# Kernel tuning notes

Measured on AMD Instinct MI355X. Metric: run time of the kernel, lower is better.

Reference implementation:

```python
import jax, jax.numpy as jnp
import numpy as np
from jax.ops import segment_sum, segment_max

N = 50000
E = 800000
F_IN = 128
F_HEAD = 32
HEADS = 8
N_CLASSES = 32
NEG_SLOPE = 0.2


def setup_inputs() -> dict:
    key = jax.random.key(0)
    ks = jax.random.split(key, 12)
    x = jax.random.normal(ks[0], (N, F_IN), dtype=jnp.float32)
    edge_index = jax.random.randint(ks[1], (2, E), 0, N, dtype=jnp.int64)
    # layer 1 params (in=128 -> heads=8, out=32)
    s1 = 1.0 / np.sqrt(F_IN)
    W1 = jax.random.uniform(ks[2], (F_IN, HEADS * F_HEAD), jnp.float32, -s1, s1)
    a_src1 = jax.random.uniform(ks[3], (HEADS, F_HEAD), jnp.float32, -s1, s1)
    a_dst1 = jax.random.uniform(ks[4], (HEADS, F_HEAD), jnp.float32, -s1, s1)
    b1 = jnp.zeros((HEADS * F_HEAD,), jnp.float32)
    # layer 2 params (in=256 -> heads=1, out=32)
    s2 = 1.0 / np.sqrt(HEADS * F_HEAD)
    W2 = jax.random.uniform(ks[5], (HEADS * F_HEAD, N_CLASSES), jnp.float32, -s2, s2)
    a_src2 = jax.random.uniform(ks[6], (1, N_CLASSES), jnp.float32, -s2, s2)
    a_dst2 = jax.random.uniform(ks[7], (1, N_CLASSES), jnp.float32, -s2, s2)
    b2 = jnp.zeros((N_CLASSES,), jnp.float32)
    return {"x": x, "edge_index": edge_index, "W1": W1, "a_src1": a_src1,
            "a_dst1": a_dst1, "b1": b1, "W2": W2, "a_src2": a_src2,
            "a_dst2": a_dst2, "b2": b2}


def gat_conv(x, W, a_src, a_dst, b, src, dst, heads, out_ch):
    n = x.shape[0]
    h = (x @ W).reshape(n, heads, out_ch)                  # [N,H,F]
    alpha_src = jnp.einsum('nhf,hf->nh', h, a_src)         # [N,H]
    alpha_dst = jnp.einsum('nhf,hf->nh', h, a_dst)
    e = alpha_src[src] + alpha_dst[dst]                    # [E,H]
    e = jnp.where(e > 0, e, NEG_SLOPE * e)                 # LeakyReLU(0.2)
    # segment softmax over edges grouped by destination node
    m = segment_max(e, dst, num_segments=n)                # [N,H]
    ex = jnp.exp(e - m[dst])
    denom = segment_sum(ex, dst, num_segments=n)           # [N,H]
    alpha = ex / (denom[dst] + 1e-16)                      # [E,H]
    out = segment_sum(alpha[:, :, None] * h[src], dst, num_segments=n)  # [N,H,F]
    return out.reshape(n, heads * out_ch) + b


def reference(x, edge_index, W1, a_src1, a_dst1, b1, W2, a_src2, a_dst2, b2):
    src, dst = edge_index[0], edge_index[1]
    h = gat_conv(x, W1, a_src1, a_dst1, b1, src, dst, HEADS, F_HEAD)
    h = jax.nn.elu(h)
    out = gat_conv(h, W2, a_src2, a_dst2, b2, src, dst, 1, N_CLASSES)
    return out
```

## Files before the change

### kernel.cpp

```cpp
#include <hip/hip_runtime.h>
#include <math.h>

#define NNODES 50000
#define NEDGES 800000
#define GB 782

typedef _Float16 f16;
typedef _Float16 f16x8 __attribute__((ext_vector_type(8)));
typedef _Float16 f16x4 __attribute__((ext_vector_type(4)));
typedef float f32x4 __attribute__((ext_vector_type(4)));
typedef float f32x8 __attribute__((ext_vector_type(8)));


__global__ __launch_bounds__(256) void k_deg_wfrag(const int* __restrict__ ei, int* __restrict__ deg,
                                                   int* __restrict__ rank,
                                                   const float* __restrict__ W1, const float* __restrict__ W2,
                                                   f16* __restrict__ W1f, f16* __restrict__ W2f) {
    int bid = blockIdx.x;
    if (bid < NEDGES / 256) {
        int e = bid * 256 + threadIdx.x;
        rank[e] = atomicAdd(&deg[ei[NEDGES + e]], 1);
    } else {
        int id = (bid - NEDGES / 256) * 256 + threadIdx.x;
        if (id < 32768) {
            int k = id >> 8, c = id & 255;
            int kc = k >> 5, quad = (k & 31) >> 3, j = k & 7;
            W1f[(((kc << 8) + c) * 4 + quad) * 8 + j] = (f16)W1[id];
        } else {
            int i2 = id - 32768;
            int k = i2 >> 5, c = i2 & 31;
            int kc = k >> 5, quad = (k & 31) >> 3, j = k & 7;
            W2f[(((kc << 5) + c) * 4 + quad) * 8 + j] = (f16)W2[i2];
        }
    }
}

__global__ __launch_bounds__(256) void k_scanA(const int* __restrict__ deg, int* __restrict__ incl,
                                               int* __restrict__ partial) {
    int t = threadIdx.x;
    int i = blockIdx.x * 256 + t;
    int v = (i < NNODES) ? deg[i] : 0;
    int lane = t & 63, wid = t >> 6;
    int s = v;
#pragma unroll
    for (int d = 1; d < 64; d <<= 1) { int u = __shfl_up(s, d, 64); if (lane >= d) s += u; }
    __shared__ int wtot[4];
    if (lane == 63) wtot[wid] = s;
    __syncthreads();
    int off = 0;
    for (int w = 0; w < wid; ++w) off += wtot[w];
    s += off;
    if (i < NNODES) incl[i] = s;
    if (t == 255) partial[blockIdx.x] = s;
}

__global__ __launch_bounds__(256) void k_scanC(const int* __restrict__ deg, const int* __restrict__ incl,
                                               const int* __restrict__ partial, int* __restrict__ rowst) {
    int t = threadIdx.x, bid = blockIdx.x;
    int v = (t < bid) ? partial[t] : 0;
    int lane = t & 63, wid = t >> 6;
#pragma unroll
    for (int d = 1; d < 64; d <<= 1) v += __shfl_xor(v, d);
    __shared__ int ws[4];
    if (lane == 0) ws[wid] = v;
    __syncthreads();
    int choff = ws[0] + ws[1] + ws[2] + ws[3];
    int i = bid * 256 + t;
    if (i < NNODES) {
        int rs1 = incl[i] + choff;
        rowst[i + 1] = rs1;
        if (i == 0) rowst[0] = 0;
    }
}


__global__ __launch_bounds__(256) void k_gemm1_sc(const float* __restrict__ X, const f16* __restrict__ W1f,
                                                  const float* __restrict__ Asrc, const float* __restrict__ Adst,
                                                  f16* __restrict__ h1h, float* __restrict__ as1,
                                                  float* __restrict__ ad1, const int* __restrict__ ei,
                                                  const int* __restrict__ rowst, const int* __restrict__ rank,
                                                  unsigned* __restrict__ sd_csr) {
    __shared__ f16 sA[64 * 136];
    int bid = blockIdx.x;
    int t = threadIdx.x;
    if (bid >= GB) {
        int e = (bid - GB) * 256 + t;
        if (e < NEDGES) {
            int s = ei[e], d = ei[NEDGES + e];
            int pos = rowst[d] + rank[e];
            sd_csr[pos] = ((unsigned)d << 16) | (unsigned)s;
        }
        return;
    }
    int bm = bid * 64;
#pragma unroll
    for (int i = 0; i < 8; ++i) {
        int idx = i * 256 + t;
        int row = idx >> 5, c4 = (idx & 31) << 2;
        int gr = bm + row;
        float4 v = make_float4(0.f, 0.f, 0.f, 0.f);
        if (gr < NNODES) v = *(const float4*)(X + (size_t)gr * 128 + c4);
        f16x4 h = {(f16)v.x, (f16)v.y, (f16)v.z, (f16)v.w};
        *(f16x4*)&sA[row * 136 + c4] = h;
    }
    __syncthreads();
    int lane = t & 63, w = t >> 6;
    int r = lane & 15, quad = lane >> 4;
    int r0 = w * 16;
    f32x4 acc[2][8];
#pragma unroll
    for (int h2 = 0; h2 < 2; ++h2)
#pragma unroll
        for (int nt = 0; nt < 8; ++nt) acc[h2][nt] = (f32x4){0.f, 0.f, 0.f, 0.f};
#pragma unroll
    for (int kc = 0; kc < 4; ++kc) {
        f16x8 a = *(f16x8*)&sA[(r0 + r) * 136 + kc * 32 + quad * 8];
#pragma unroll
        for (int h2 = 0; h2 < 2; ++h2)
#pragma unroll
            for (int nt = 0; nt < 8; ++nt) {
                f16x8 b = *(const f16x8*)&W1f[(((kc << 8) + h2 * 128 + nt * 16 + r) * 4 + quad) * 8];
                acc[h2][nt] = __builtin_amdgcn_mfma_f32_16x16x32_f16(a, b, acc[h2][nt], 0, 0, 0);
            }
    }
#pragma unroll
    for (int h2 = 0; h2 < 2; ++h2)
#pragma unroll
        for (int nt = 0; nt < 8; ++nt)
#pragma unroll
            for (int i = 0; i < 4; ++i) {
                int gr = bm + r0 + quad * 4 + i;
                if (gr < NNODES) h1h[(size_t)gr * 256 + h2 * 128 + nt * 16 + r] = (f16)acc[h2][nt][i];
            }
#pragma unroll
    for (int h2 = 0; h2 < 2; ++h2) {
        float asv[8], adv[8];
#pragma unroll
        for (int nt = 0; nt < 8; ++nt) {
            asv[nt] = Asrc[h2 * 128 + nt * 16 + r];
            adv[nt] = Adst[h2 * 128 + nt * 16 + r];
        }
#pragma unroll
        for (int i = 0; i < 4; ++i) {
            int gr = bm + r0 + quad * 4 + i;
#pragma unroll
            for (int hl = 0; hl < 4; ++hl) {
                float ps = acc[h2][2 * hl][i] * asv[2 * hl] + acc[h2][2 * hl + 1][i] * asv[2 * hl + 1];
                float pd = acc[h2][2 * hl][i] * adv[2 * hl] + acc[h2][2 * hl + 1][i] * adv[2 * hl + 1];
#pragma unroll
                for (int off = 1; off < 16; off <<= 1) {
                    ps += __shfl_xor(ps, off);
                    pd += __shfl_xor(pd, off);
                }
                if (r == 0 && gr < NNODES) {
                    as1[(size_t)gr * 8 + h2 * 4 + hl] = ps;
                    ad1[(size_t)gr * 8 + h2 * 4 + hl] = pd;
                }
            }
        }
    }
}

__global__ __launch_bounds__(256) void k_gemm2(const f16* __restrict__ h2h, const f16* __restrict__ W2f,
                                               const float* __restrict__ Asrc, const float* __restrict__ Adst,
                                               f16* __restrict__ gh, float* __restrict__ as2,
                                               float* __restrict__ ad2) {
    int t = threadIdx.x;
    int bm = blockIdx.x * 64;
    int lane = t & 63, w = t >> 6;
    int r = lane & 15, quad = lane >> 4;
    int r0 = w * 16;
    int gra = bm + r0 + r;
    int grac = gra < NNODES ? gra : 0;
    f32x4 acc[2];
    acc[0] = (f32x4){0.f, 0.f, 0.f, 0.f};
    acc[1] = (f32x4){0.f, 0.f, 0.f, 0.f};
#pragma unroll
    for (int kc = 0; kc < 8; ++kc) {
        f16x8 a = *(const f16x8*)(h2h + (size_t)grac * 256 + kc * 32 + quad * 8);
#pragma unroll
        for (int nt = 0; nt < 2; ++nt) {
            f16x8 b = *(const f16x8*)&W2f[(((kc << 5) + nt * 16 + r) * 4 + quad) * 8];
            acc[nt] = __builtin_amdgcn_mfma_f32_16x16x32_f16(a, b, acc[nt], 0, 0, 0);
        }
    }
#pragma unroll
    for (int nt = 0; nt < 2; ++nt)
#pragma unroll
        for (int i = 0; i < 4; ++i) {
            int gr = bm + r0 + quad * 4 + i;
            if (gr < NNODES) gh[(size_t)gr * 32 + nt * 16 + r] = (f16)acc[nt][i];
        }
    float as0 = Asrc[r], as16 = Asrc[16 + r];
    float ad0 = Adst[r], ad16 = Adst[16 + r];
#pragma unroll
    for (int i = 0; i < 4; ++i) {
        int gr = bm + r0 + quad * 4 + i;
        float ps = acc[0][i] * as0 + acc[1][i] * as16;
        float pd = acc[0][i] * ad0 + acc[1][i] * ad16;
#pragma unroll
        for (int off = 1; off < 16; off <<= 1) {
            ps += __shfl_xor(ps, off);
            pd += __shfl_xor(pd, off);
        }
        if (r == 0 && gr < NNODES) { as2[gr] = ps; ad2[gr] = pd; }
    }
}


__global__ __launch_bounds__(256) void k_agg1(const int* __restrict__ rowst, const unsigned* __restrict__ sd_csr,
                                              const float* __restrict__ as1, const float* __restrict__ ad1,
                                              const f16* __restrict__ h1h, const float* __restrict__ b1,
                                              f16* __restrict__ h2h, f16* __restrict__ eh) {
    int w = threadIdx.x >> 6, lane = threadIdx.x & 63;
    int n = blockIdx.x * 4 + w;
    int s = rowst[n], e = rowst[n + 1];
    int head8 = lane & 7, slot8 = lane >> 3;
    float adn = ad1[(size_t)n * 8 + head8];
    float sum = 0.f;
    for (int j = s + slot8; j < e; j += 8) {
        int src = (int)(sd_csr[j] & 0xffffu);
        float x = as1[(size_t)src * 8 + head8] + adn;
        x = x > 0.f ? x : 0.2f * x;
        float ex = __expf(x);
        eh[(size_t)j * 8 + head8] = (f16)ex;
        sum += ex;
    }
    sum += __shfl_xor(sum, 8);
    sum += __shfl_xor(sum, 16);
    sum += __shfl_xor(sum, 32);
    float inv = 1.f / (sum + 1e-16f);
    asm volatile("s_waitcnt vmcnt(0) lgkmcnt(0)" ::: "memory");
    int slot = lane >> 5;
    int ch32 = lane & 31;
    int c0 = ch32 << 3;
    int hm = ch32 >> 2;
    float invq = __shfl(inv, hm);
    const f16* __restrict__ hp = h1h + c0;
    const f16* __restrict__ ep = eh + hm;
    f32x8 acc = (f32x8){0.f, 0.f, 0.f, 0.f, 0.f, 0.f, 0.f, 0.f};
    int j = s + slot;
    for (; j + 6 < e; j += 8) {
        int s0 = (int)(sd_csr[j] & 0xffffu),     s1 = (int)(sd_csr[j + 2] & 0xffffu);
        int s2 = (int)(sd_csr[j + 4] & 0xffffu), s3 = (int)(sd_csr[j + 6] & 0xffffu);
        float a0 = (float)ep[(size_t)j * 8] * invq;
        float a1 = (float)ep[(size_t)(j + 2) * 8] * invq;
        float a2 = (float)ep[(size_t)(j + 4) * 8] * invq;
        float a3 = (float)ep[(size_t)(j + 6) * 8] * invq;
        f16x8 v0 = *(const f16x8*)(hp + (size_t)s0 * 256);
        f16x8 v1 = *(const f16x8*)(hp + (size_t)s1 * 256);
        f16x8 v2 = *(const f16x8*)(hp + (size_t)s2 * 256);
        f16x8 v3 = *(const f16x8*)(hp + (size_t)s3 * 256);
#pragma unroll
        for (int k = 0; k < 8; ++k)
            acc[k] += a0 * (float)v0[k] + a1 * (float)v1[k] + a2 * (float)v2[k] + a3 * (float)v3[k];
    }
    for (; j < e; j += 2) {
        int s0 = (int)(sd_csr[j] & 0xffffu);
        float a0 = (float)ep[(size_t)j * 8] * invq;
        f16x8 v0 = *(const f16x8*)(hp + (size_t)s0 * 256);
#pragma unroll
        for (int k = 0; k < 8; ++k) acc[k] += a0 * (float)v0[k];
    }
#pragma unroll
    for (int k = 0; k < 8; ++k) acc[k] += __shfl_xor(acc[k], 32);
    if (slot == 0) {
        float4 b0 = *(const float4*)(b1 + c0);
        float4 b4 = *(const float4*)(b1 + c0 + 4);
        float o[8] = {acc[0] + b0.x, acc[1] + b0.y, acc[2] + b0.z, acc[3] + b0.w,
                      acc[4] + b4.x, acc[5] + b4.y, acc[6] + b4.z, acc[7] + b4.w};
        f16x8 oh;
#pragma unroll
        for (int k = 0; k < 8; ++k) {
            float v = o[k];
            v = v > 0.f ? v : __expf(v) - 1.f;
            oh[k] = (f16)v;
        }
        *(f16x8*)(h2h + (size_t)n * 256 + c0) = oh;
    }
}

__global__ __launch_bounds__(256) void k_agg2(const int* __restrict__ rowst, const unsigned* __restrict__ sd_csr,
                                              const float* __restrict__ as2, const float* __restrict__ ad2,
                                              const f16* __restrict__ gh, const float* __restrict__ b2,
                                              float* __restrict__ out) {
    int w = threadIdx.x >> 6, lane = threadIdx.x & 63;
    int n = blockIdx.x * 4 + w;
    int s = rowst[n], e = rowst[n + 1];
    float adn = ad2[n];
    float sum = 0.f;
    for (int j = s + lane; j < e; j += 64) {
        float x = as2[(int)(sd_csr[j] & 0xffffu)] + adn;
        x = x > 0.f ? x : 0.2f * x;
        sum += __expf(x);
    }
#pragma unroll
    for (int d = 1; d < 64; d <<= 1) sum += __shfl_xor(sum, d);
    float inv = 1.f / (sum + 1e-16f);
    int slot = lane >> 5, c = lane & 31;
    const f16* __restrict__ gp = gh + c;
    float acc = 0.f;
    for (int j = s + slot; j < e; j += 2) {
        int sn = (int)(sd_csr[j] & 0xffffu);
        float x = as2[sn] + adn;
        x = x > 0.f ? x : 0.2f * x;
        acc += __expf(x) * inv * (float)gp[(size_t)sn * 32];
    }
    acc += __shfl_xor(acc, 32);
    if (slot == 0) out[(size_t)n * 32 + c] = acc + b2[c];
}


extern "C" void kernel_launch(void* const* d_in, const int* in_sizes, int n_in,
                              void* d_out, int out_size, void* d_ws, size_t ws_size,
                              hipStream_t stream) {
    const float* x    = (const float*)d_in[0];
    const int*   ei   = (const int*)d_in[1];
    const float* W1   = (const float*)d_in[2];
    const float* As1  = (const float*)d_in[3];
    const float* Ad1  = (const float*)d_in[4];
    const float* b1   = (const float*)d_in[5];
    const float* W2   = (const float*)d_in[6];
    const float* As2  = (const float*)d_in[7];
    const float* Ad2  = (const float*)d_in[8];
    const float* b2   = (const float*)d_in[9];
    float* out = (float*)d_out;

    char* p = (char*)d_ws;
    auto alloc = [&](size_t bytes) -> char* {
        char* r = p;
        p += (bytes + 255) & ~(size_t)255;
        return r;
    };
    f16* h1h      = (f16*)alloc((size_t)NNODES * 256 * 2);
    f16* h2h      = (f16*)alloc((size_t)NNODES * 256 * 2);
    f16* W1f      = (f16*)alloc((size_t)128 * 256 * 2);
    f16* W2f      = (f16*)alloc((size_t)256 * 32 * 2);
    f16* gh       = (f16*)alloc((size_t)NNODES * 32 * 2);
    f16* eh       = (f16*)alloc((size_t)NEDGES * 8 * 2);
    float* asrc1  = (float*)alloc((size_t)NNODES * 8 * 4);
    float* adst1  = (float*)alloc((size_t)NNODES * 8 * 4);
    float* asrc2  = (float*)alloc((size_t)NNODES * 4);
    float* adst2  = (float*)alloc((size_t)NNODES * 4);
    int* deg      = (int*)alloc((size_t)NNODES * 4);
    int* incl     = (int*)alloc((size_t)NNODES * 4);
    int* rowst    = (int*)alloc((size_t)(NNODES + 1) * 4);
    int* rank     = (int*)alloc((size_t)NEDGES * 4);
    unsigned* sdc = (unsigned*)alloc((size_t)NEDGES * 4);
    int* partial  = (int*)alloc(256 * 4);

    const int EB = NEDGES / 256;
    const int NCH = (NNODES + 255) / 256;

    hipMemsetAsync(deg, 0, (size_t)NNODES * 4, stream);
    k_deg_wfrag<<<EB + 160, 256, 0, stream>>>(ei, deg, rank, W1, W2, W1f, W2f);
    k_scanA<<<NCH, 256, 0, stream>>>(deg, incl, partial);
    k_scanC<<<NCH, 256, 0, stream>>>(deg, incl, partial, rowst);

    k_gemm1_sc<<<GB + EB, 256, 0, stream>>>(x, W1f, As1, Ad1, h1h, asrc1, adst1, ei, rowst, rank, sdc);
    k_agg1<<<NNODES / 4, 256, 0, stream>>>(rowst, sdc, asrc1, adst1, h1h, b1, h2h, eh);

    k_gemm2<<<(NNODES + 63) / 64, 256, 0, stream>>>(h2h, W2f, As2, Ad2, gh, asrc2, adst2);
    k_agg2<<<NNODES / 4, 256, 0, stream>>>(rowst, sdc, asrc2, adst2, gh, b2, out);
}
```

Before: 298.3 us.

## Fuse softmax denominator into single-pass GAT aggregation, drop edge-weight buffer

Both aggregation kernels now compute exp-scores and the softmax denominator in the same loop that accumulates weighted neighbor features, normalizing once at the end instead of running a separate pass. This removes the f16 per-edge exp buffer in layer 1 (its writes, reads and the wait barrier) and the duplicate score pass in layer 2. Layer 2 also packs two channels per lane with four edge slots to widen loads. The cost is redundant exp and gather of attention scores per lane (each of 4 lanes per head recomputes it), and no max subtraction, as before.

Result: faster. 267.0 us (-10.5%).

```diff
diff --git a/kernel.cpp b/kernel.cpp
--- a/kernel.cpp
+++ b/kernel.cpp
@@ -8,6 +8,7 @@
 typedef _Float16 f16;
 typedef _Float16 f16x8 __attribute__((ext_vector_type(8)));
 typedef _Float16 f16x4 __attribute__((ext_vector_type(4)));
+typedef _Float16 f16x2 __attribute__((ext_vector_type(2)));
 typedef float f32x4 __attribute__((ext_vector_type(4)));
 typedef float f32x8 __attribute__((ext_vector_type(8)));
 
@@ -211,64 +212,60 @@
 __global__ __launch_bounds__(256) void k_agg1(const int* __restrict__ rowst, const unsigned* __restrict__ sd_csr,
                                               const float* __restrict__ as1, const float* __restrict__ ad1,
                                               const f16* __restrict__ h1h, const float* __restrict__ b1,
-                                              f16* __restrict__ h2h, f16* __restrict__ eh) {
+                                              f16* __restrict__ h2h) {
     int w = threadIdx.x >> 6, lane = threadIdx.x & 63;
     int n = blockIdx.x * 4 + w;
     int s = rowst[n], e = rowst[n + 1];
-    int head8 = lane & 7, slot8 = lane >> 3;
-    float adn = ad1[(size_t)n * 8 + head8];
-    float sum = 0.f;
-    for (int j = s + slot8; j < e; j += 8) {
-        int src = (int)(sd_csr[j] & 0xffffu);
-        float x = as1[(size_t)src * 8 + head8] + adn;
-        x = x > 0.f ? x : 0.2f * x;
-        float ex = __expf(x);
-        eh[(size_t)j * 8 + head8] = (f16)ex;
-        sum += ex;
-    }
-    sum += __shfl_xor(sum, 8);
-    sum += __shfl_xor(sum, 16);
-    sum += __shfl_xor(sum, 32);
-    float inv = 1.f / (sum + 1e-16f);
-    asm volatile("s_waitcnt vmcnt(0) lgkmcnt(0)" ::: "memory");
     int slot = lane >> 5;
     int ch32 = lane & 31;
     int c0 = ch32 << 3;
     int hm = ch32 >> 2;
-    float invq = __shfl(inv, hm);
+    float adn = ad1[(size_t)n * 8 + hm];
     const f16* __restrict__ hp = h1h + c0;
-    const f16* __restrict__ ep = eh + hm;
+    const float* __restrict__ ap = as1 + hm;
     f32x8 acc = (f32x8){0.f, 0.f, 0.f, 0.f, 0.f, 0.f, 0.f, 0.f};
+    float sum = 0.f;
     int j = s + slot;
     for (; j + 6 < e; j += 8) {
         int s0 = (int)(sd_csr[j] & 0xffffu),     s1 = (int)(sd_csr[j + 2] & 0xffffu);
         int s2 = (int)(sd_csr[j + 4] & 0xffffu), s3 = (int)(sd_csr[j + 6] & 0xffffu);
-        float a0 = (float)ep[(size_t)j * 8] * invq;
-        float a1 = (float)ep[(size_t)(j + 2) * 8] * invq;
-        float a2 = (float)ep[(size_t)(j + 4) * 8] * invq;
-        float a3 = (float)ep[(size_t)(j + 6) * 8] * invq;
+        float x0 = ap[(size_t)s0 * 8] + adn;
+        float x1 = ap[(size_t)s1 * 8] + adn;
+        float x2 = ap[(size_t)s2 * 8] + adn;
+        float x3 = ap[(size_t)s3 * 8] + adn;
         f16x8 v0 = *(const f16x8*)(hp + (size_t)s0 * 256);
         f16x8 v1 = *(const f16x8*)(hp + (size_t)s1 * 256);
         f16x8 v2 = *(const f16x8*)(hp + (size_t)s2 * 256);
         f16x8 v3 = *(const f16x8*)(hp + (size_t)s3 * 256);
+        x0 = fmaxf(x0, 0.2f * x0);
+        x1 = fmaxf(x1, 0.2f * x1);
+        x2 = fmaxf(x2, 0.2f * x2);
+        x3 = fmaxf(x3, 0.2f * x3);
+        float e0 = __expf(x0), e1 = __expf(x1), e2 = __expf(x2), e3 = __expf(x3);
+        sum += (e0 + e1) + (e2 + e3);
 #pragma unroll
         for (int k = 0; k < 8; ++k)
-            acc[k] += a0 * (float)v0[k] + a1 * (float)v1[k] + a2 * (float)v2[k] + a3 * (float)v3[k];
+            acc[k] += e0 * (float)v0[k] + e1 * (float)v1[k] + e2 * (float)v2[k] + e3 * (float)v3[k];
     }
     for (; j < e; j += 2) {
         int s0 = (int)(sd_csr[j] & 0xffffu);
-        float a0 = (float)ep[(size_t)j * 8] * invq;
+        float x0 = ap[(size_t)s0 * 8] + adn;
         f16x8 v0 = *(const f16x8*)(hp + (size_t)s0 * 256);
-#pragma unroll
-        for (int k = 0; k < 8; ++k) acc[k] += a0 * (float)v0[k];
-    }
+        x0 = fmaxf(x0, 0.2f * x0);
+        float e0 = __expf(x0);
+        sum += e0;
+#pragma unroll
+        for (int k = 0; k < 8; ++k) acc[k] += e0 * (float)v0[k];
+    }
+    sum += __shfl_xor(sum, 32);
 #pragma unroll
     for (int k = 0; k < 8; ++k) acc[k] += __shfl_xor(acc[k], 32);
     if (slot == 0) {
+        float inv = 1.f / (sum + 1e-16f);
         float4 b0 = *(const float4*)(b1 + c0);
         float4 b4 = *(const float4*)(b1 + c0 + 4);
-        float o[8] = {acc[0] + b0.x, acc[1] + b0.y, acc[2] + b0.z, acc[3] + b0.w,
-                      acc[4] + b4.x, acc[5] + b4.y, acc[6] + b4.z, acc[7] + b4.w};
+        float o[8] = {acc[0] * inv + b0.x, acc[1] * inv + b0.y, acc[2] * inv + b0.z, acc[3] * inv + b0.w,
+                      acc[4] * inv + b4.x, acc[5] * inv + b4.y, acc[6] * inv + b4.z, acc[7] * inv + b4.w};
         f16x8 oh;
 #pragma unroll
         for (int k = 0; k < 8; ++k) {
@@ -287,27 +284,48 @@
     int w = threadIdx.x >> 6, lane = threadIdx.x & 63;
     int n = blockIdx.x * 4 + w;
     int s = rowst[n], e = rowst[n + 1];
+    int slot = lane >> 4;
+    int cp = lane & 15;
     float adn = ad2[n];
-    float sum = 0.f;
-    for (int j = s + lane; j < e; j += 64) {
-        float x = as2[(int)(sd_csr[j] & 0xffffu)] + adn;
-        x = x > 0.f ? x : 0.2f * x;
-        sum += __expf(x);
-    }
-#pragma unroll
-    for (int d = 1; d < 64; d <<= 1) sum += __shfl_xor(sum, d);
-    float inv = 1.f / (sum + 1e-16f);
-    int slot = lane >> 5, c = lane & 31;
-    const f16* __restrict__ gp = gh + c;
-    float acc = 0.f;
-    for (int j = s + slot; j < e; j += 2) {
-        int sn = (int)(sd_csr[j] & 0xffffu);
-        float x = as2[sn] + adn;
-        x = x > 0.f ? x : 0.2f * x;
-        acc += __expf(x) * inv * (float)gp[(size_t)sn * 32];
-    }
-    acc += __shfl_xor(acc, 32);
-    if (slot == 0) out[(size_t)n * 32 + c] = acc + b2[c];
+    const f16* __restrict__ gp = gh + 2 * cp;
+    float a0 = 0.f, a1 = 0.f, sum = 0.f;
+    int j = s + slot;
+    for (; j + 4 < e; j += 8) {
+        int s0 = (int)(sd_csr[j] & 0xffffu);
+        int s1 = (int)(sd_csr[j + 4] & 0xffffu);
+        float x0 = as2[s0] + adn, x1 = as2[s1] + adn;
+        f16x2 v0 = *(const f16x2*)(gp + (size_t)s0 * 32);
+        f16x2 v1 = *(const f16x2*)(gp + (size_t)s1 * 32);
+        x0 = fmaxf(x0, 0.2f * x0);
+        x1 = fmaxf(x1, 0.2f * x1);
+        float e0 = __expf(x0), e1 = __expf(x1);
+        sum += e0 + e1;
+        a0 += e0 * (float)v0[0] + e1 * (float)v1[0];
+        a1 += e0 * (float)v0[1] + e1 * (float)v1[1];
+    }
+    for (; j < e; j += 4) {
+        int s0 = (int)(sd_csr[j] & 0xffffu);
+        float x0 = as2[s0] + adn;
+        f16x2 v0 = *(const f16x2*)(gp + (size_t)s0 * 32);
+        x0 = fmaxf(x0, 0.2f * x0);
+        float e0 = __expf(x0);
+        sum += e0;
+        a0 += e0 * (float)v0[0];
+        a1 += e0 * (float)v0[1];
+    }
+#pragma unroll
+    for (int d = 16; d < 64; d <<= 1) {
+        sum += __shfl_xor(sum, d);
+        a0 += __shfl_xor(a0, d);
+        a1 += __shfl_xor(a1, d);
+    }
+    if (slot == 0) {
+        float inv = 1.f / (sum + 1e-16f);
+        float2 o;
+        o.x = a0 * inv + b2[2 * cp];
+        o.y = a1 * inv + b2[2 * cp + 1];
+        *(float2*)(out + (size_t)n * 32 + 2 * cp) = o;
+    }
 }
 
 
@@ -337,7 +355,6 @@
     f16* W1f      = (f16*)alloc((size_t)128 * 256 * 2);
     f16* W2f      = (f16*)alloc((size_t)256 * 32 * 2);
     f16* gh       = (f16*)alloc((size_t)NNODES * 32 * 2);
-    f16* eh       = (f16*)alloc((size_t)NEDGES * 8 * 2);
     float* asrc1  = (float*)alloc((size_t)NNODES * 8 * 4);
     float* adst1  = (float*)alloc((size_t)NNODES * 8 * 4);
     float* asrc2  = (float*)alloc((size_t)NNODES * 4);
@@ -358,7 +375,7 @@
     k_scanC<<<NCH, 256, 0, stream>>>(deg, incl, partial, rowst);
 
     k_gemm1_sc<<<GB + EB, 256, 0, stream>>>(x, W1f, As1, Ad1, h1h, asrc1, adst1, ei, rowst, rank, sdc);
-    k_agg1<<<NNODES / 4, 256, 0, stream>>>(rowst, sdc, asrc1, adst1, h1h, b1, h2h, eh);
+    k_agg1<<<NNODES / 4, 256, 0, stream>>>(rowst, sdc, asrc1, adst1, h1h, b1, h2h);
 
     k_gemm2<<<(NNODES + 63) / 64, 256, 0, stream>>>(h2h, W2f, As2, Ad2, gh, asrc2, adst2);
     k_agg2<<<NNODES / 4, 256, 0, stream>>>(rowst, sdc, asrc2, adst2, gh, b2, out);
```
